# Optimization experiments

Hardware: AMD Instinct MI355X
Metric: run time of the kernel (lower is better)

The kernel has to match this reference:

```python
import jax, jax.numpy as jnp
import numpy as np
import math

B, T, C = 2, 4096, 768
NH = 12
HS = C // NH

def setup_inputs() -> dict:
    key = jax.random.key(0)
    k1, k2, k3 = jax.random.split(key, 3)
    x = jax.random.normal(k1, (B, T, C), dtype=jnp.float32)
    w_attn = jax.random.normal(k2, (C, 3 * C), dtype=jnp.float32) * (1.0 / math.sqrt(C))
    w_proj = jax.random.normal(k3, (C, C), dtype=jnp.float32) * (1.0 / math.sqrt(C))
    return {"x": x, "w_attn": w_attn, "w_proj": w_proj}

def reference(x, w_attn, w_proj):
    b, t, c = x.shape
    qkv = x @ w_attn                      # [b, t, 3c]
    q, k, v = jnp.split(qkv, 3, axis=-1)
    # [b, nh, t, hs]
    q = q.reshape(b, t, NH, HS).transpose(0, 2, 1, 3)
    k = k.reshape(b, t, NH, HS).transpose(0, 2, 1, 3)
    v = v.reshape(b, t, NH, HS).transpose(0, 2, 1, 3)
    scores = jnp.einsum('bhqd,bhkd->bhqk', q, k) / math.sqrt(HS)
    causal = jnp.tril(jnp.ones((t, t), dtype=bool))
    scores = jnp.where(causal[None, None], scores, -jnp.inf)
    att = jax.nn.softmax(scores, axis=-1)  # dropout p=0 -> identity
    out = jnp.einsum('bhqk,bhkd->bhqd', att, v)
    out = out.transpose(0, 2, 1, 3).reshape(b, t, c)
    return out @ w_proj
```

## Files before the change

### kernel.cpp

```cpp
#include <hip/hip_runtime.h>
#include <hip/hip_bf16.h>
#include <stdint.h>

#define NB 2
#define NT 4096
#define NC 768
#define NHEAD 12
#define HS 64
#define MTOK (NB * NT)
#define C3 (3 * NC)
#define CQK (2 * NC)

typedef __bf16 bf16x8 __attribute__((ext_vector_type(8)));
typedef float f32x4 __attribute__((ext_vector_type(4)));
typedef float f32x16 __attribute__((ext_vector_type(16)));

#define KSCALE_LOG2E 0.18033688011f

__device__ __forceinline__ unsigned short f2bf(float f) {
  union { float f; uint32_t u; } v; v.f = f;
  uint32_t r = v.u + 0x7fffu + ((v.u >> 16) & 1u);
  return (unsigned short)(r >> 16);
}
__device__ __forceinline__ unsigned short bft(float f) {
  return (unsigned short)(__builtin_bit_cast(unsigned int, f) >> 16);
}
__device__ __forceinline__ uint32_t pack_bf2(float a, float b) {
  return __builtin_amdgcn_perm(__builtin_bit_cast(uint32_t, a),
                               __builtin_bit_cast(uint32_t, b), 0x03020706u);
}

__device__ __forceinline__ void gload_lds16(const unsigned short* g, unsigned short* ldsbase) {
  __builtin_amdgcn_global_load_lds(
      (const __attribute__((address_space(1))) unsigned int*)g,
      (__attribute__((address_space(3))) unsigned int*)ldsbase, 16, 0, 0);
}

__device__ __forceinline__ f32x4 mfma16(bf16x8 a, bf16x8 b, f32x4 c) {
  return __builtin_amdgcn_mfma_f32_16x16x32_bf16(a, b, c, 0, 0, 0);
}
__device__ __forceinline__ f32x16 mfma32(bf16x8 a, bf16x8 b, f32x16 c) {
  return __builtin_amdgcn_mfma_f32_32x32x16_bf16(a, b, c, 0, 0, 0);
}

__global__ __launch_bounds__(256) void prep(
    const float* __restrict__ x, const float* __restrict__ wa, const float* __restrict__ wp,
    unsigned short* __restrict__ xb, unsigned short* __restrict__ waT,
    unsigned short* __restrict__ wpT) {
  const int bx = blockIdx.x;
  if (bx < 576) {
    __shared__ float tile[64][65];
    const float* src; unsigned short* dst;
    int srcN, dstN, k0, n0, qscale;
    if (bx < 432) {
      src = wa; dst = waT; srcN = C3; dstN = NC; qscale = 1;
      k0 = (bx / 36) * 64; n0 = (bx % 36) * 64;
    } else {
      const int t = bx - 432;
      src = wp; dst = wpT; srcN = NC; dstN = NC; qscale = 0;
      k0 = (t / 12) * 64; n0 = (t % 12) * 64;
    }
    const int tr = threadIdx.x >> 4;
    const int tc = (threadIdx.x & 15) * 4;
#pragma unroll
    for (int p = 0; p < 4; ++p) {
      const int r = p * 16 + tr;
      const float4 v = *reinterpret_cast<const float4*>(src + (size_t)(k0 + r) * srcN + n0 + tc);
      tile[r][tc + 0] = v.x; tile[r][tc + 1] = v.y;
      tile[r][tc + 2] = v.z; tile[r][tc + 3] = v.w;
    }
    __syncthreads();
#pragma unroll
    for (int p = 0; p < 4; ++p) {
      const int n = p * 16 + tr;
      const float sc = (qscale && (n0 + n) < NC) ? KSCALE_LOG2E : 1.0f;
      ushort4 o;
      o.x = f2bf(tile[tc + 0][n] * sc); o.y = f2bf(tile[tc + 1][n] * sc);
      o.z = f2bf(tile[tc + 2][n] * sc); o.w = f2bf(tile[tc + 3][n] * sc);
      *reinterpret_cast<ushort4*>(dst + (size_t)(n0 + n) * dstN + k0 + tc) = o;
    }
  } else {
    const int gid = (bx - 576) * 256 + threadIdx.x;
    const float4 v = reinterpret_cast<const float4*>(x)[gid];
    ushort4 o;
    o.x = f2bf(v.x); o.y = f2bf(v.y); o.z = f2bf(v.z); o.w = f2bf(v.w);
    reinterpret_cast<ushort4*>(xb)[gid] = o;
  }
}

template <int OUT_BF16>
__global__ __launch_bounds__(256) void gemm128(
    const unsigned short* __restrict__ A,
    const unsigned short* __restrict__ Bt,
    void* __restrict__ Cout,
    unsigned short* __restrict__ vT,
    int M, int N, int K, int ldc) {
  __shared__ unsigned short smem[2 * 128 * 64];
  unsigned short* As = smem;
  unsigned short* Bs = smem + 128 * 64;

  const int tid = threadIdx.x;
  const int wave = tid >> 6;
  const int lane = tid & 63;
  const int li = lane & 15;
  const int lq = lane >> 4;
  const int wm = wave & 1;
  const int wn = wave >> 1;
  const int row0 = blockIdx.y * 128;
  const int col0 = blockIdx.x * 128;

  const int crow = lane >> 3;
  const int cchunk = ((lane & 7) ^ crow) * 8;

  f32x4 acc[4][4] = {};

  for (int k0 = 0; k0 < K; k0 += 64) {
#pragma unroll
    for (int i = 0; i < 4; ++i) {
      const int R = wave * 32 + i * 8;
      gload_lds16(A + (size_t)(row0 + R + crow) * K + k0 + cchunk, &As[R * 64]);
      gload_lds16(Bt + (size_t)(col0 + R + crow) * K + k0 + cchunk, &Bs[R * 64]);
    }
    __syncthreads();

#pragma unroll
    for (int ks = 0; ks < 2; ++ks) {
      bf16x8 af[4], bf[4];
#pragma unroll
      for (int f = 0; f < 4; ++f) {
        const int arow = wm * 64 + f * 16 + li;
        af[f] = *reinterpret_cast<const bf16x8*>(&As[arow * 64 + (((ks * 4 + lq) ^ (li & 7)) << 3)]);
        const int brow = wn * 64 + f * 16 + li;
        bf[f] = *reinterpret_cast<const bf16x8*>(&Bs[brow * 64 + (((ks * 4 + lq) ^ (li & 7)) << 3)]);
      }
#pragma unroll
      for (int fa = 0; fa < 4; ++fa)
#pragma unroll
        for (int fb = 0; fb < 4; ++fb)
          acc[fa][fb] = mfma16(af[fa], bf[fb], acc[fa][fb]);
    }
    __syncthreads();
  }

  if (OUT_BF16) {
    if (col0 >= 2 * NC) {
      const int b = row0 >> 12;
      const int t0r = row0 & (NT - 1);
      const int h0 = (col0 - 2 * NC) >> 6;
#pragma unroll
      for (int fa = 0; fa < 4; ++fa) {
#pragma unroll
        for (int fb = 0; fb < 4; ++fb) {
          const int cc = wn * 64 + fb * 16 + li;
#pragma unroll
          for (int r = 0; r < 4; ++r) {
            const int tt = wm * 64 + fa * 16 + lq * 4 + r;
            const int slot = cc * 16 + ((tt >> 3) ^ (cc & 15));
            smem[slot * 8 + (tt & 7)] = f2bf(acc[fa][fb][r]);
          }
        }
      }
      __syncthreads();
      const int ch = tid & 15;
#pragma unroll
      for (int j = 0; j < 8; ++j) {
        const int cc = (tid >> 4) + 16 * j;
        const uint4 v = *reinterpret_cast<const uint4*>(
            smem + (size_t)(cc * 16 + (ch ^ (cc & 15))) * 8);
        const int bh = b * NHEAD + h0 + (cc >> 6);
        const int d = cc & 63;
        *reinterpret_cast<uint4*>(vT + (size_t)bh * HS * NT + (size_t)d * NT + t0r + ch * 8) = v;
      }
    } else {
      unsigned short* Cb = (unsigned short*)Cout;
#pragma unroll
      for (int fa = 0; fa < 4; ++fa) {
        const int gr = row0 + wm * 64 + fa * 16 + lq * 4;
#pragma unroll
        for (int fb = 0; fb < 4; ++fb) {
          const int gc = col0 + wn * 64 + fb * 16 + li;
#pragma unroll
          for (int r = 0; r < 4; ++r)
            Cb[(size_t)(gr + r) * ldc + gc] = f2bf(acc[fa][fb][r]);
        }
      }
    }
  } else {
    float* Cf = (float*)Cout;
#pragma unroll
    for (int fa = 0; fa < 4; ++fa) {
      const int gr = row0 + wm * 64 + fa * 16 + lq * 4;
#pragma unroll
      for (int fb = 0; fb < 4; ++fb) {
        const int gc = col0 + wn * 64 + fb * 16 + li;
#pragma unroll
        for (int r = 0; r < 4; ++r)
          Cf[(size_t)(gr + r) * ldc + gc] = acc[fa][fb][r];
      }
    }
  }
}


__global__ __launch_bounds__(256) void attn(
    const unsigned short* __restrict__ qkv,
    const unsigned short* __restrict__ vT,
    float* __restrict__ OpartA,
    float* __restrict__ OpartB,
    float* __restrict__ laccA,
    float* __restrict__ laccB) {
  __shared__ unsigned short Ks[3][64 * 64];
  __shared__ unsigned short Vts[3][64 * 64];

  const int tid = threadIdx.x;
  const int wave = tid >> 6;
  const int lane = tid & 63;
  const int l31 = lane & 31;
  const int lh = lane >> 5;
  const int sw = l31 & 7;

  const int bid = (int)blockIdx.x;
  const int xcd = bid & 7;
  const int wl = bid >> 3;
  const int grp = xcd * 3 + wl % 3;
  const int rank = wl / 3;
  const int qi = 31 - (rank >> 1);
  const int part = rank & 1;
  const int nt = 2 * qi + 2;
  const int tauS = part ? 0 : (qi + 1);
  const int tauE = part ? (qi + 1) : nt;
  const int b = grp / 12;
  const int h = grp - b * 12;
  const int q0 = qi * 128;
  const int bh = grp;

  const size_t baseQ = (size_t)b * NT * CQK + (size_t)h * HS;
  const size_t baseK = baseQ + NC;
  const unsigned short* kq = qkv + baseK;
  const unsigned short* vbase = vT + (size_t)bh * HS * NT;

  const int qw = q0 + wave * 32;
  const int qtok = qw + l31;

  bf16x8 bq[4];
#pragma unroll
  for (int ks = 0; ks < 4; ++ks)
    bq[ks] = *reinterpret_cast<const bf16x8*>(
        qkv + baseQ + (size_t)(qw + l31) * CQK + ks * 16 + lh * 8);

  bf16x8 vones;
#pragma unroll
  for (int i = 0; i < 8; ++i) vones[i] = (__bf16)1.0f;

  f32x16 o0 = {}, o1 = {}, la = {};
  const f32x16 zf = {};

  const int grow = lane >> 3;
  const int gch = (lane & 7) ^ grow;
  const int wr0 = wave * 8;
  const int wr1 = wave * 8 + 32;

#define STAGE(TAU, BUFI)                                                        \
  do {                                                                          \
    const int t0s_ = (TAU) * 64;                                                \
    gload_lds16(kq + (size_t)(t0s_ + wr0 + grow) * CQK + gch * 8,               \
                &Ks[BUFI][wr0 * 64]);                                           \
    gload_lds16(kq + (size_t)(t0s_ + wr1 + grow) * CQK + gch * 8,               \
                &Ks[BUFI][wr1 * 64]);                                           \
    gload_lds16(vbase + (size_t)(wr0 + grow) * NT + t0s_ + gch * 8,             \
                &Vts[BUFI][wr0 * 64]);                                          \
    gload_lds16(vbase + (size_t)(wr1 + grow) * NT + t0s_ + gch * 8,             \
                &Vts[BUFI][wr1 * 64]);                                          \
  } while (0)

#define EXP_PACK(ST, KBLK, DOMASK)                                             \
  do {                                                                         \
    const int kb_ = t0 + (KBLK) * 32 + 4 * lh;                                 \
    float p_[16];                                                              \
    _Pragma("unroll") for (int r = 0; r < 16; ++r) {                           \
      float v_ = (ST)[r];                                                      \
      if (DOMASK) {                                                            \
        const int kt_ = kb_ + (r & 3) + 8 * (r >> 2);                          \
        if (kt_ > qtok) v_ = -INFINITY;                                        \
      }                                                                        \
      p_[r] = __builtin_amdgcn_exp2f(v_);                                      \
    }                                                                          \
    _Pragma("unroll") for (int s = 0; s < 2; ++s) {                            \
      uint32_t a_ = pack_bf2(p_[8 * s + 0], p_[8 * s + 1]);                    \
      uint32_t b_ = pack_bf2(p_[8 * s + 2], p_[8 * s + 3]);                    \
      uint32_t c_ = pack_bf2(p_[8 * s + 4], p_[8 * s + 5]);                    \
      uint32_t d_ = pack_bf2(p_[8 * s + 6], p_[8 * s + 7]);                    \
      asm("v_permlane32_swap_b32 %0, %1" : "+v"(a_), "+v"(c_));                \
      asm("v_permlane32_swap_b32 %0, %1" : "+v"(b_), "+v"(d_));                \
      union { uint32_t u[4]; bf16x8 v8; } pu_;                                 \
      pu_.u[0] = a_; pu_.u[1] = b_; pu_.u[2] = c_; pu_.u[3] = d_;              \
      pa[2 * (KBLK) + s] = pu_.v8;                                             \
    }                                                                          \
  } while (0)

#define PV_STEP(KS)                                                            \
  do {                                                                         \
    const int off_ = ((((KS) * 2 + lh) ^ sw) << 3);                            \
    const bf16x8 bv0_ =                                                        \
        *reinterpret_cast<const bf16x8*>(Vc + (size_t)l31 * 64 + off_);        \
    const bf16x8 bv1_ =                                                        \
        *reinterpret_cast<const bf16x8*>(Vc + (size_t)(32 + l31) * 64 + off_); \
    la = mfma32(pa[KS], vones, la);                                            \
    o0 = mfma32(pa[KS], bv0_, o0);                                             \
    o1 = mfma32(pa[KS], bv1_, o1);                                             \
  } while (0)

  STAGE(tauS, 0);
  STAGE(tauS + 1, 1);

  int cur = 0;
  for (int tau = tauS; tau < tauE; ++tau) {
    const int t0 = tau * 64;
    if (tau + 1 < tauE) asm volatile("s_waitcnt vmcnt(4)" ::: "memory");
    else                asm volatile("s_waitcnt vmcnt(0)" ::: "memory");
    __builtin_amdgcn_s_barrier();
    __builtin_amdgcn_sched_barrier(0);
    if (tau + 2 < tauE) {
      int nb = cur + 2; if (nb >= 3) nb -= 3;
      STAGE(tau + 2, nb);
    }

    const unsigned short* Kc = Ks[cur];
    const unsigned short* Vc = Vts[cur];

    if (t0 <= qw + 31) {
      const bool act1 = (t0 + 32 <= qw + 31);
      const bool m0 = (t0 + 31 > qw);
      const bool m1 = (t0 + 63 > qw);

      f32x16 st0, st1;
      __builtin_amdgcn_s_setprio(1);
      {
        const bf16x8 ka0 = *reinterpret_cast<const bf16x8*>(
            Kc + (size_t)l31 * 64 + ((lh ^ sw) << 3));
        st0 = mfma32(ka0, bq[0], zf);
      }
#pragma unroll
      for (int ks = 1; ks < 4; ++ks) {
        const bf16x8 ka = *reinterpret_cast<const bf16x8*>(
            Kc + (size_t)l31 * 64 + (((ks * 2 + lh) ^ sw) << 3));
        st0 = mfma32(ka, bq[ks], st0);
      }
      if (act1) {
        {
          const bf16x8 ka0 = *reinterpret_cast<const bf16x8*>(
              Kc + (size_t)(32 + l31) * 64 + ((lh ^ sw) << 3));
          st1 = mfma32(ka0, bq[0], zf);
        }
#pragma unroll
        for (int ks = 1; ks < 4; ++ks) {
          const bf16x8 ka = *reinterpret_cast<const bf16x8*>(
              Kc + (size_t)(32 + l31) * 64 + (((ks * 2 + lh) ^ sw) << 3));
          st1 = mfma32(ka, bq[ks], st1);
        }
      }
      __builtin_amdgcn_s_setprio(0);

      bf16x8 pa[4];
      if (m0) EXP_PACK(st0, 0, 1); else EXP_PACK(st0, 0, 0);
      if (act1) {
        if (m1) EXP_PACK(st1, 1, 1); else EXP_PACK(st1, 1, 0);
      }

      __builtin_amdgcn_s_setprio(1);
      PV_STEP(0); PV_STEP(1);
      if (act1) { PV_STEP(2); PV_STEP(3); }
      __builtin_amdgcn_s_setprio(0);
    }
    ++cur; if (cur == 3) cur = 0;
  }
#undef STAGE
#undef EXP_PACK
#undef PV_STEP

  float* slotO = part ? OpartB : OpartA;
  float* lrow = (part ? laccB : laccA) + (size_t)bh * NT;
#pragma unroll
  for (int r = 0; r < 16; ++r) {
    const int q = qw + (r & 3) + 8 * (r >> 2) + 4 * lh;
    if (l31 == 0) lrow[q] = la[r];
    float* orow = slotO + ((size_t)b * NT + q) * NC + h * HS;
    orow[l31] = o0[r];
    orow[32 + l31] = o1[r];
  }
}

__global__ __launch_bounds__(256) void finalize(
    const float* __restrict__ OpartA, const float* __restrict__ OpartB,
    const float* __restrict__ laccA, const float* __restrict__ laccB,
    unsigned short* __restrict__ aob) {
  const int idx4 = (blockIdx.x * 256 + threadIdx.x);
  if (idx4 >= MTOK * NC / 4) return;
  const int idx = idx4 * 4;
  const int row = idx / NC;
  const int cc = idx - row * NC;
  const int b = row >> 12;
  const int t = row & (NT - 1);
  const int h = cc >> 6;
  const size_t lofs = (size_t)(b * NHEAD + h) * NT + t;
  const float inv = 1.0f / (laccA[lofs] + laccB[lofs]);
  const float4 v0 = *reinterpret_cast<const float4*>(OpartA + (size_t)idx);
  const float4 v1 = *reinterpret_cast<const float4*>(OpartB + (size_t)idx);
  ushort4 o;
  o.x = bft((v0.x + v1.x) * inv); o.y = bft((v0.y + v1.y) * inv);
  o.z = bft((v0.z + v1.z) * inv); o.w = bft((v0.w + v1.w) * inv);
  reinterpret_cast<ushort4*>(aob)[idx4] = o;
}

extern "C" void kernel_launch(void* const* d_in, const int* in_sizes, int n_in,
                              void* d_out, int out_size, void* d_ws, size_t ws_size,
                              hipStream_t stream) {
  const float* x = (const float*)d_in[0];
  const float* w_attn = (const float*)d_in[1];
  const float* w_proj = (const float*)d_in[2];
  float* outp = (float*)d_out;

  char* w = (char*)d_ws;
  float* OpartA = (float*)w;
  unsigned short* xb = (unsigned short*)w;
  unsigned short* waT = xb + (size_t)MTOK * NC;
  float* laccA = OpartA + (size_t)MTOK * NC;
  float* laccB = laccA + (size_t)NB * NHEAD * NT;
  unsigned short* qkvb = (unsigned short*)(laccB + (size_t)NB * NHEAD * NT);
  unsigned short* aob  = qkvb + (size_t)MTOK * CQK;
  unsigned short* vTb  = aob + (size_t)MTOK * NC;
  unsigned short* wpT  = vTb + (size_t)MTOK * NC;

  prep<<<576 + MTOK * NC / 4 / 256, 256, 0, stream>>>(x, w_attn, w_proj, xb, waT, wpT);

  gemm128<1><<<dim3(C3 / 128, MTOK / 128), 256, 0, stream>>>(
      xb, waT, qkvb, vTb, MTOK, C3, NC, CQK);

  attn<<<1536, 256, 0, stream>>>(qkvb, vTb, OpartA, outp, laccA, laccB);

  finalize<<<(MTOK * NC / 4 + 255) / 256, 256, 0, stream>>>(OpartA, outp, laccA, laccB, aob);

  gemm128<0><<<dim3(NC / 128, MTOK / 128), 256, 0, stream>>>(
      aob, wpT, outp, nullptr, MTOK, NC, NC, NC);
}
```

Before: 229.4 us.

## Pair complementary attention segments per block and remap GEMM tiles across XCDs

The attention kernel now launches half as many blocks, and each block runs two work segments in sequence: a segment for query tile qi and another for tile 31-qi. This balances causal work per block and lowers the block count from 1536 to 768. Both GEMM launches switch to a 1D grid whose block index is remapped so consecutive tiles land on the same XCD, aiming for better L2 reuse. The paired segments add a __syncthreads between them and lengthen each block's run, and the serial dependency cuts latency overlap between independent blocks.

New measurement: 247.9 us. 8.0% more time.

```diff
diff --git a/kernel.cpp b/kernel.cpp
--- a/kernel.cpp
+++ b/kernel.cpp
@@ -94,7 +94,7 @@
     const unsigned short* __restrict__ Bt,
     void* __restrict__ Cout,
     unsigned short* __restrict__ vT,
-    int M, int N, int K, int ldc) {
+    int M, int N, int K, int ldc, int nx) {
   __shared__ unsigned short smem[2 * 128 * 64];
   unsigned short* As = smem;
   unsigned short* Bs = smem + 128 * 64;
@@ -106,8 +106,14 @@
   const int lq = lane >> 4;
   const int wm = wave & 1;
   const int wn = wave >> 1;
-  const int row0 = blockIdx.y * 128;
-  const int col0 = blockIdx.x * 128;
+
+  const int bid = (int)blockIdx.x;
+  const int nwg = (int)gridDim.x;
+  const int w = (bid & 7) * (nwg >> 3) + (bid >> 3);
+  const int cx = w % nx;
+  const int cy = w / nx;
+  const int row0 = cy * 128;
+  const int col0 = cx * 128;
 
   const int crow = lane >> 3;
   const int cchunk = ((lane & 7) ^ crow) * 8;
@@ -223,15 +229,9 @@
   const int xcd = bid & 7;
   const int wl = bid >> 3;
   const int grp = xcd * 3 + wl % 3;
-  const int rank = wl / 3;
-  const int qi = 31 - (rank >> 1);
-  const int part = rank & 1;
-  const int nt = 2 * qi + 2;
-  const int tauS = part ? 0 : (qi + 1);
-  const int tauE = part ? (qi + 1) : nt;
+  const int qia = 31 - wl / 3;
   const int b = grp / 12;
   const int h = grp - b * 12;
-  const int q0 = qi * 128;
   const int bh = grp;
 
   const size_t baseQ = (size_t)b * NT * CQK + (size_t)h * HS;
@@ -239,20 +239,9 @@
   const unsigned short* kq = qkv + baseK;
   const unsigned short* vbase = vT + (size_t)bh * HS * NT;
 
-  const int qw = q0 + wave * 32;
-  const int qtok = qw + l31;
-
-  bf16x8 bq[4];
-#pragma unroll
-  for (int ks = 0; ks < 4; ++ks)
-    bq[ks] = *reinterpret_cast<const bf16x8*>(
-        qkv + baseQ + (size_t)(qw + l31) * CQK + ks * 16 + lh * 8);
-
   bf16x8 vones;
 #pragma unroll
   for (int i = 0; i < 8; ++i) vones[i] = (__bf16)1.0f;
-
-  f32x16 o0 = {}, o1 = {}, la = {};
   const f32x16 zf = {};
 
   const int grow = lane >> 3;
@@ -310,84 +299,105 @@
     o1 = mfma32(pa[KS], bv1_, o1);                                             \
   } while (0)
 
-  STAGE(tauS, 0);
-  STAGE(tauS + 1, 1);
-
-  int cur = 0;
-  for (int tau = tauS; tau < tauE; ++tau) {
-    const int t0 = tau * 64;
-    if (tau + 1 < tauE) asm volatile("s_waitcnt vmcnt(4)" ::: "memory");
-    else                asm volatile("s_waitcnt vmcnt(0)" ::: "memory");
-    __builtin_amdgcn_s_barrier();
-    __builtin_amdgcn_sched_barrier(0);
-    if (tau + 2 < tauE) {
-      int nb = cur + 2; if (nb >= 3) nb -= 3;
-      STAGE(tau + 2, nb);
-    }
-
-    const unsigned short* Kc = Ks[cur];
-    const unsigned short* Vc = Vts[cur];
-
-    if (t0 <= qw + 31) {
-      const bool act1 = (t0 + 32 <= qw + 31);
-      const bool m0 = (t0 + 31 > qw);
-      const bool m1 = (t0 + 63 > qw);
-
-      f32x16 st0, st1;
-      __builtin_amdgcn_s_setprio(1);
-      {
-        const bf16x8 ka0 = *reinterpret_cast<const bf16x8*>(
-            Kc + (size_t)l31 * 64 + ((lh ^ sw) << 3));
-        st0 = mfma32(ka0, bq[0], zf);
-      }
-#pragma unroll
-      for (int ks = 1; ks < 4; ++ks) {
-        const bf16x8 ka = *reinterpret_cast<const bf16x8*>(
-            Kc + (size_t)l31 * 64 + (((ks * 2 + lh) ^ sw) << 3));
-        st0 = mfma32(ka, bq[ks], st0);
-      }
-      if (act1) {
+  for (int seg = 0; seg < 2; ++seg) {
+    const int part = seg;
+    const int qi = part ? (31 - qia) : qia;
+    const int q0 = qi * 128;
+    const int tauS = part ? 0 : (qi + 1);
+    const int tauE = part ? (qi + 1) : (2 * qi + 2);
+
+    const int qw = q0 + wave * 32;
+    const int qtok = qw + l31;
+
+    bf16x8 bq[4];
+#pragma unroll
+    for (int ks = 0; ks < 4; ++ks)
+      bq[ks] = *reinterpret_cast<const bf16x8*>(
+          qkv + baseQ + (size_t)(qw + l31) * CQK + ks * 16 + lh * 8);
+
+    f32x16 o0 = {}, o1 = {}, la = {};
+
+    if (seg) __syncthreads();
+
+    STAGE(tauS, 0);
+    STAGE(tauS + 1, 1);
+
+    int cur = 0;
+    for (int tau = tauS; tau < tauE; ++tau) {
+      const int t0 = tau * 64;
+      if (tau + 1 < tauE) asm volatile("s_waitcnt vmcnt(4)" ::: "memory");
+      else                asm volatile("s_waitcnt vmcnt(0)" ::: "memory");
+      __builtin_amdgcn_s_barrier();
+      __builtin_amdgcn_sched_barrier(0);
+      if (tau + 2 < tauE) {
+        int nb = cur + 2; if (nb >= 3) nb -= 3;
+        STAGE(tau + 2, nb);
+      }
+
+      const unsigned short* Kc = Ks[cur];
+      const unsigned short* Vc = Vts[cur];
+
+      if (t0 <= qw + 31) {
+        const bool act1 = (t0 + 32 <= qw + 31);
+        const bool m0 = (t0 + 31 > qw);
+        const bool m1 = (t0 + 63 > qw);
+
+        f32x16 st0, st1;
+        __builtin_amdgcn_s_setprio(1);
         {
           const bf16x8 ka0 = *reinterpret_cast<const bf16x8*>(
-              Kc + (size_t)(32 + l31) * 64 + ((lh ^ sw) << 3));
-          st1 = mfma32(ka0, bq[0], zf);
+              Kc + (size_t)l31 * 64 + ((lh ^ sw) << 3));
+          st0 = mfma32(ka0, bq[0], zf);
         }
 #pragma unroll
         for (int ks = 1; ks < 4; ++ks) {
           const bf16x8 ka = *reinterpret_cast<const bf16x8*>(
-              Kc + (size_t)(32 + l31) * 64 + (((ks * 2 + lh) ^ sw) << 3));
-          st1 = mfma32(ka, bq[ks], st1);
-        }
-      }
-      __builtin_amdgcn_s_setprio(0);
-
-      bf16x8 pa[4];
-      if (m0) EXP_PACK(st0, 0, 1); else EXP_PACK(st0, 0, 0);
-      if (act1) {
-        if (m1) EXP_PACK(st1, 1, 1); else EXP_PACK(st1, 1, 0);
-      }
-
-      __builtin_amdgcn_s_setprio(1);
-      PV_STEP(0); PV_STEP(1);
-      if (act1) { PV_STEP(2); PV_STEP(3); }
-      __builtin_amdgcn_s_setprio(0);
-    }
-    ++cur; if (cur == 3) cur = 0;
+              Kc + (size_t)l31 * 64 + (((ks * 2 + lh) ^ sw) << 3));
+          st0 = mfma32(ka, bq[ks], st0);
+        }
+        if (act1) {
+          {
+            const bf16x8 ka0 = *reinterpret_cast<const bf16x8*>(
+                Kc + (size_t)(32 + l31) * 64 + ((lh ^ sw) << 3));
+            st1 = mfma32(ka0, bq[0], zf);
+          }
+#pragma unroll
+          for (int ks = 1; ks < 4; ++ks) {
+            const bf16x8 ka = *reinterpret_cast<const bf16x8*>(
+                Kc + (size_t)(32 + l31) * 64 + (((ks * 2 + lh) ^ sw) << 3));
+            st1 = mfma32(ka, bq[ks], st1);
+          }
+        }
+        __builtin_amdgcn_s_setprio(0);
+
+        bf16x8 pa[4];
+        if (m0) EXP_PACK(st0, 0, 1); else EXP_PACK(st0, 0, 0);
+        if (act1) {
+          if (m1) EXP_PACK(st1, 1, 1); else EXP_PACK(st1, 1, 0);
+        }
+
+        __builtin_amdgcn_s_setprio(1);
+        PV_STEP(0); PV_STEP(1);
+        if (act1) { PV_STEP(2); PV_STEP(3); }
+        __builtin_amdgcn_s_setprio(0);
+      }
+      ++cur; if (cur == 3) cur = 0;
+    }
+
+    float* slotO = part ? OpartB : OpartA;
+    float* lrow = (part ? laccB : laccA) + (size_t)bh * NT;
+#pragma unroll
+    for (int r = 0; r < 16; ++r) {
+      const int q = qw + (r & 3) + 8 * (r >> 2) + 4 * lh;
+      if (l31 == 0) lrow[q] = la[r];
+      float* orow = slotO + ((size_t)b * NT + q) * NC + h * HS;
+      orow[l31] = o0[r];
+      orow[32 + l31] = o1[r];
+    }
   }
 #undef STAGE
 #undef EXP_PACK
 #undef PV_STEP
-
-  float* slotO = part ? OpartB : OpartA;
-  float* lrow = (part ? laccB : laccA) + (size_t)bh * NT;
-#pragma unroll
-  for (int r = 0; r < 16; ++r) {
-    const int q = qw + (r & 3) + 8 * (r >> 2) + 4 * lh;
-    if (l31 == 0) lrow[q] = la[r];
-    float* orow = slotO + ((size_t)b * NT + q) * NC + h * HS;
-    orow[l31] = o0[r];
-    orow[32 + l31] = o1[r];
-  }
 }
 
 __global__ __launch_bounds__(256) void finalize(
@@ -433,13 +443,13 @@
 
   prep<<<576 + MTOK * NC / 4 / 256, 256, 0, stream>>>(x, w_attn, w_proj, xb, waT, wpT);
 
-  gemm128<1><<<dim3(C3 / 128, MTOK / 128), 256, 0, stream>>>(
-      xb, waT, qkvb, vTb, MTOK, C3, NC, CQK);
-
-  attn<<<1536, 256, 0, stream>>>(qkvb, vTb, OpartA, outp, laccA, laccB);
+  gemm128<1><<<1152, 256, 0, stream>>>(
+      xb, waT, qkvb, vTb, MTOK, C3, NC, CQK, C3 / 128);
+
+  attn<<<768, 256, 0, stream>>>(qkvb, vTb, OpartA, outp, laccA, laccB);
 
   finalize<<<(MTOK * NC / 4 + 255) / 256, 256, 0, stream>>>(OpartA, outp, laccA, laccB, aob);
 
-  gemm128<0><<<dim3(NC / 128, MTOK / 128), 256, 0, stream>>>(
-      aob, wpT, outp, nullptr, MTOK, NC, NC, NC);
-}
+  gemm128<0><<<384, 256, 0, stream>>>(
+      aob, wpT, outp, nullptr, MTOK, NC, NC, NC, NC / 128);
+}
```
